# Kernel optimization log

Measured on AMD Instinct MI355X. Metric: run time of the kernel, lower is better.

The kernel has to match this reference:

```python
import jax, jax.numpy as jnp
import numpy as np

B, N, C = 8, 1024, 768
H, D = 12, 64
SCALE = D ** -0.5
EPS = 1e-5

def layernorm(x, g, b):
    mu = jnp.mean(x, axis=-1, keepdims=True)
    var = jnp.var(x, axis=-1, keepdims=True)
    return (x - mu) * jax.lax.rsqrt(var + EPS) * g + b

def setup_inputs() -> dict:
    key = jax.random.key(0)
    ks = jax.random.split(key, 5)
    return {
        "x": jax.random.normal(ks[0], (B, N, C), jnp.float32),
        "qkv_w": jax.random.normal(ks[1], (3 * C, C), jnp.float32) * 0.02,
        "qkv_b": jax.random.normal(ks[2], (3 * C,), jnp.float32) * 0.02,
        "qn_g": jnp.ones((D,), jnp.float32),
        "qn_b": jnp.zeros((D,), jnp.float32),
        "kn_g": jnp.ones((D,), jnp.float32),
        "kn_b": jnp.zeros((D,), jnp.float32),
        "proj_w": jax.random.normal(ks[3], (C, C), jnp.float32) * 0.02,
        "proj_b": jnp.zeros((C,), jnp.float32),
    }

def reference(x, qkv_w, qkv_b, qn_g, qn_b, kn_g, kn_b, proj_w, proj_b):
    # qkv projection: [B,N,3C] -> [3,B,H,N,D]
    qkv = jnp.einsum('bnc,oc->bno', x, qkv_w) + qkv_b
    qkv = qkv.reshape(B, N, 3, H, D).transpose(2, 0, 3, 1, 4)
    q, k, v = qkv[0], qkv[1], qkv[2]
    q = layernorm(q, qn_g, qn_b) * SCALE
    k = layernorm(k, kn_g, kn_b)
    # explicit attention matrix [B,H,N,N] (module stores it)
    attn = jax.nn.softmax(jnp.einsum('bhqd,bhkd->bhqk', q, k), axis=-1)
    out = jnp.einsum('bhqk,bhkd->bhqd', attn, v)
    out = out.transpose(0, 2, 1, 3).reshape(B, N, C)
    out = jnp.einsum('bnc,oc->bno', out, proj_w) + proj_b
    return out
```

## Files before the change

### kernel.cpp

```cpp
#include <hip/hip_runtime.h>
#include <cstdint>

#define Bz 8
#define Nn 1024
#define Cc 768
#define Hh 12
#define Dd 64
#define C3 2304
#define BN 8192

constexpr float EPS = 1e-5f;
constexpr float QSCALE = 0.125f * 1.44269504088896340736f;

typedef __attribute__((ext_vector_type(8))) short bf16x8;
typedef _Float16 f16x8 __attribute__((ext_vector_type(8)));
typedef __attribute__((ext_vector_type(4))) float f32x4;
typedef __attribute__((ext_vector_type(16))) float f32x16;

__device__ __forceinline__ short f2b(float f) {
    union { float f; unsigned u; } x; x.f = f;
    unsigned r = x.u + 0x7FFFu + ((x.u >> 16) & 1u);
    return (short)(r >> 16);
}
__device__ __forceinline__ unsigned cvtpk(float a, float b) {
    unsigned r;
    asm("v_cvt_pk_bf16_f32 %0, %1, %2" : "=v"(r) : "v"(a), "v"(b));
    return r;
}

__device__ __forceinline__ f32x4 MFMAH(f16x8 a, f16x8 b, f32x4 c) {
    return __builtin_amdgcn_mfma_f32_16x16x32_f16(a, b, c, 0, 0, 0);
}
__device__ __forceinline__ f32x16 MFMA32(bf16x8 a, bf16x8 b, f32x16 c) {
    return __builtin_amdgcn_mfma_f32_32x32x16_bf16(a, b, c, 0, 0, 0);
}
__device__ __forceinline__ f16x8 ldf16(const _Float16* p) { return *(const f16x8*)p; }
__device__ __forceinline__ void gld16(const void* g, void* l) {
    __builtin_amdgcn_global_load_lds((const __attribute__((address_space(1))) unsigned int*)g,
                                     (__attribute__((address_space(3))) unsigned int*)(l),
                                     16, 0, 0);
}

__global__ __launch_bounds__(256) void cvt_all(
    const float* __restrict__ x, const float* __restrict__ wq, const float* __restrict__ wp,
    _Float16* __restrict__ xh, _Float16* __restrict__ wqh, _Float16* __restrict__ wph)
{
    const int n1 = BN * Cc / 8, n2 = n1 + C3 * Cc / 8, n3 = n2 + Cc * Cc / 8;
    int i = blockIdx.x * 256 + threadIdx.x;
    const float* s; _Float16* d; int off;
    if (i < n1)      { s = x;  d = xh;  off = i; }
    else if (i < n2) { s = wq; d = wqh; off = i - n1; }
    else if (i < n3) { s = wp; d = wph; off = i - n2; }
    else return;
    float4 a = *(const float4*)(s + (size_t)off * 8);
    float4 b = *(const float4*)(s + (size_t)off * 8 + 4);
    f16x8 o;
    o[0] = (_Float16)a.x; o[1] = (_Float16)a.y; o[2] = (_Float16)a.z; o[3] = (_Float16)a.w;
    o[4] = (_Float16)b.x; o[5] = (_Float16)b.y; o[6] = (_Float16)b.z; o[7] = (_Float16)b.w;
    *(f16x8*)(d + (size_t)off * 8) = o;
}

template<int EPI>
__global__ __launch_bounds__(256, 4) void gemm_f16(
    const _Float16* __restrict__ A,
    const _Float16* __restrict__ W,
    const float* __restrict__ bias,
    float* __restrict__ Out,
    short* __restrict__ qp, short* __restrict__ kp, short* __restrict__ vp,
    const float* __restrict__ qg, const float* __restrict__ qb,
    const float* __restrict__ kg, const float* __restrict__ kb,
    int nx)
{
    __shared__ _Float16 As[128 * 64];
    __shared__ _Float16 Bs[128 * 64];
    const int tid = threadIdx.x;
    const int lane = tid & 63;
    const int w = tid >> 6;
    const int wr = w >> 1, wc = w & 1;
    const int l15 = lane & 15, l4 = lane >> 4;
    const int lr = lane >> 3;
    const int lslot = lane & 7;

    const int chunk = gridDim.x >> 3;
    const int wg = (blockIdx.x & 7) * chunk + (blockIdx.x >> 3);
    const int by = wg / nx;
    int bx = wg % nx;
    if (by & 1) bx = nx - 1 - bx;
    const int m0 = by * 128;
    const int n0 = bx * 128;

    auto stage = [&](int kt) {
        const int k0 = kt * 64;
#pragma unroll
        for (int j = 0; j < 8; ++j) {
            int i = w * 8 + j;
            int isA = (i < 16);
            int ib = isA ? i : i - 16;
            int row = ib * 8 + lr;
            int gslot = lslot ^ (row & 7);
            const _Float16* src = (isA ? A + (size_t)(m0 + row) * 768
                                       : W + (size_t)(n0 + row) * 768) + k0 + gslot * 8;
            _Float16* dst = (isA ? As : Bs) + ib * 512;
            gld16(src, dst);
        }
    };

    f32x4 acc[4][4];
#pragma unroll
    for (int mi = 0; mi < 4; ++mi)
#pragma unroll
        for (int ni = 0; ni < 4; ++ni) { acc[mi][ni][0]=0.f; acc[mi][ni][1]=0.f; acc[mi][ni][2]=0.f; acc[mi][ni][3]=0.f; }

    stage(0);
    for (int kt = 0; kt < 12; ++kt) {
        __syncthreads();
#pragma unroll
        for (int ks = 0; ks < 2; ++ks) {
            f16x8 af[4], bfr[4];
#pragma unroll
            for (int mi = 0; mi < 4; ++mi) {
                int row = wr * 64 + mi * 16 + l15;
                int slot = (ks * 4 + l4) ^ (row & 7);
                af[mi] = ldf16(&As[row * 64 + slot * 8]);
            }
#pragma unroll
            for (int ni = 0; ni < 4; ++ni) {
                int row = wc * 64 + ni * 16 + l15;
                int slot = (ks * 4 + l4) ^ (row & 7);
                bfr[ni] = ldf16(&Bs[row * 64 + slot * 8]);
            }
#pragma unroll
            for (int mi = 0; mi < 4; ++mi)
#pragma unroll
                for (int ni = 0; ni < 4; ++ni)
                    acc[mi][ni] = MFMAH(af[mi], bfr[ni], acc[mi][ni]);
        }
        __syncthreads();
        if (kt < 11) stage(kt + 1);
    }

    if (EPI == 0) {
#pragma unroll
        for (int mi = 0; mi < 4; ++mi)
#pragma unroll
            for (int r = 0; r < 4; ++r) {
                int row = m0 + wr * 64 + mi * 16 + l4 * 4 + r;
#pragma unroll
                for (int ni = 0; ni < 4; ++ni) {
                    int col = n0 + wc * 64 + ni * 16 + l15;
                    Out[(size_t)row * Cc + col] = acc[mi][ni][r] + bias[col];
                }
            }
    } else {
        const int ncol0 = n0 + wc * 64;
        const int type = ncol0 / Cc;
        const int h = (ncol0 % Cc) >> 6;
        const float* gptr = (type == 0) ? qg : kg;
        const float* bptr = (type == 0) ? qb : kb;
        float biasv[4], gv[4], bv[4];
#pragma unroll
        for (int ni = 0; ni < 4; ++ni) {
            int d = ni * 16 + l15;
            biasv[ni] = bias[ncol0 + d];
            if (type < 2) { gv[ni] = gptr[d]; bv[ni] = bptr[d]; }
        }
        short* plane = (type == 0) ? qp : (type == 1) ? kp : vp;
#pragma unroll
        for (int mi = 0; mi < 4; ++mi)
#pragma unroll
            for (int r = 0; r < 4; ++r) {
                float v[4];
#pragma unroll
                for (int ni = 0; ni < 4; ++ni) v[ni] = acc[mi][ni][r] + biasv[ni];
                int row = m0 + wr * 64 + mi * 16 + l4 * 4 + r;
                size_t base = ((size_t)row * Hh + h) * 64;
                if (type < 2) {
                    float s = v[0] + v[1] + v[2] + v[3];
#pragma unroll
                    for (int off = 1; off < 16; off <<= 1) s += __shfl_xor(s, off);
                    float mu = s * (1.0f / 64.0f);
                    float s2 = 0.f;
#pragma unroll
                    for (int ni = 0; ni < 4; ++ni) { float dv = v[ni] - mu; s2 += dv * dv; }
#pragma unroll
                    for (int off = 1; off < 16; off <<= 1) s2 += __shfl_xor(s2, off);
                    float inv = rsqrtf(s2 * (1.0f / 64.0f) + EPS);
#pragma unroll
                    for (int ni = 0; ni < 4; ++ni) {
                        float rr = (v[ni] - mu) * inv * gv[ni] + bv[ni];
                        if (type == 0) rr *= QSCALE;
                        plane[base + ni * 16 + l15] = f2b(rr);
                    }
                } else {
#pragma unroll
                    for (int ni = 0; ni < 4; ++ni)
                        plane[base + ni * 16 + l15] = f2b(v[ni]);
                }
            }
    }
}

__global__ __launch_bounds__(256, 4) void flash_attn_mfma(
    const short* __restrict__ qp, const short* __restrict__ kp, const short* __restrict__ vp,
    _Float16* __restrict__ att)
{
    __shared__ short kls[2][64 * 64];
    __shared__ short vtl[2][64 * 64];
    const int tid = threadIdx.x;
    const int lane = tid & 63;
    const int w = tid >> 6;
    const int l31 = lane & 31;
    const int hi = lane >> 5;
    const int lr = lane >> 3;
    const int lslot = lane & 7;
    const int bid = (blockIdx.x & 7) * 96 + (blockIdx.x >> 3);
    const int qt = bid & 7;
    const int bh = bid >> 3;
    const int h = bh % Hh;
    const int b = bh / Hh;
    const int q0 = qt * 128;
    const size_t hbase = ((size_t)b * Nn * Hh + h) * 64;
    const int n0v = (tid & 31) * 2, d0v = (tid >> 5) * 8;
    const int khalf = n0v & 31;
    const int t2v = n0v >> 5;
    const int ksig = khalf ^ ((((khalf >> 2) ^ (khalf >> 3)) & 1) * 12);
    const int colv = t2v * 32 + ksig;

    bf16x8 qf[4];
    {
        const short* qsrc = qp + hbase + (size_t)(q0 + w * 32 + l31) * 768 + hi * 8;
#pragma unroll
        for (int ds = 0; ds < 4; ++ds)
            qf[ds] = *(const bf16x8*)(qsrc + ds * 16);
    }

    auto kstage = [&](int kt, int buf) {
#pragma unroll
        for (int i = 0; i < 2; ++i) {
            int row = i * 32 + w * 8 + lr;
            gld16(kp + hbase + (size_t)(kt * 64 + row) * 768 + (lslot ^ lr) * 8,
                  &kls[buf][(i * 32 + w * 8) * 64]);
        }
    };
    auto vcommit = [&](int buf, bf16x8 a0, bf16x8 a1) {
#pragma unroll
        for (int j = 0; j < 8; ++j) {
            int d = d0v + j;
            int fv = (d ^ (d >> 3)) & 7;
            unsigned pku = (unsigned short)a0[j] | ((unsigned)(unsigned short)a1[j] << 16);
            *(unsigned*)&vtl[buf][d * 64 + (((colv >> 3) ^ fv) << 3) + (colv & 7)] = pku;
        }
    };

    kstage(0, 0);
    {
        const short* s0 = vp + hbase + (size_t)n0v * 768 + d0v;
        vcommit(0, *(const bf16x8*)s0, *(const bf16x8*)(s0 + 768));
    }
    __syncthreads();

    f32x16 o0, o1;
#pragma unroll
    for (int i = 0; i < 16; ++i) { o0[i] = 0.f; o1[i] = 0.f; }
    float lrun = 0.f;

    for (int kt = 0; kt < 16; ++kt) {
        const int cur = kt & 1, nxt = cur ^ 1;
        bf16x8 va0, va1;
        if (kt < 15) {
            kstage(kt + 1, nxt);
            const short* s0 = vp + hbase + (size_t)((kt + 1) * 64 + n0v) * 768 + d0v;
            va0 = *(const bf16x8*)s0;
            va1 = *(const bf16x8*)(s0 + 768);
        }
        unsigned pk[2][8];
#pragma unroll
        for (int t2 = 0; t2 < 2; ++t2) {
            f32x16 st;
#pragma unroll
            for (int i = 0; i < 16; ++i) st[i] = 0.f;
            const int row = t2 * 32 + l31;
            __builtin_amdgcn_s_setprio(1);
#pragma unroll
            for (int ds = 0; ds < 4; ++ds) {
                bf16x8 kf = *(const bf16x8*)&kls[cur][row * 64 + (((ds * 2 + hi) ^ (row & 7)) << 3)];
                st = MFMA32(kf, qf[ds], st);
            }
            __builtin_amdgcn_s_setprio(0);
#pragma unroll
            for (int i = 0; i < 16; ++i) st[i] = exp2f(st[i]);
            {
                float s01 = (st[0] + st[1]) + (st[2] + st[3]);
                float s23 = (st[4] + st[5]) + (st[6] + st[7]);
                float s45 = (st[8] + st[9]) + (st[10] + st[11]);
                float s67 = (st[12] + st[13]) + (st[14] + st[15]);
                lrun += (s01 + s23) + (s45 + s67);
            }
#pragma unroll
            for (int i = 0; i < 8; ++i) pk[t2][i] = cvtpk(st[2 * i], st[2 * i + 1]);
        }
        __builtin_amdgcn_s_setprio(1);
#pragma unroll
        for (int t2 = 0; t2 < 2; ++t2)
#pragma unroll
            for (int c = 0; c < 2; ++c) {
                union { bf16x8 v; unsigned u[4]; } a;
                a.u[0] = pk[t2][c * 4 + 0]; a.u[1] = pk[t2][c * 4 + 1];
                a.u[2] = pk[t2][c * 4 + 2]; a.u[3] = pk[t2][c * 4 + 3];
#pragma unroll
                for (int nt = 0; nt < 2; ++nt) {
                    int r = nt * 32 + l31;
                    int fv = (r ^ (r >> 3)) & 7;
                    bf16x8 vf = *(const bf16x8*)&vtl[cur][r * 64 + (((t2 * 4 + c * 2 + hi) ^ fv) << 3)];
                    if (nt == 0) o0 = MFMA32(a.v, vf, o0);
                    else         o1 = MFMA32(a.v, vf, o1);
                }
            }
        __builtin_amdgcn_s_setprio(0);
        if (kt < 15) vcommit(nxt, va0, va1);
        __syncthreads();
    }

    lrun += __shfl_xor(lrun, 32);
    float linv = 1.0f / lrun;
#pragma unroll
    for (int r = 0; r < 16; ++r) {
        int qr = (r & 3) + 8 * (r >> 2) + 4 * hi;
        float invr = __shfl(linv, qr);
        int row = q0 + w * 32 + qr;
        _Float16* dst = att + (size_t)(b * Nn + row) * Cc + h * 64 + l31;
        dst[0]  = (_Float16)(o0[r] * invr);
        dst[32] = (_Float16)(o1[r] * invr);
    }
}

extern "C" void kernel_launch(void* const* d_in, const int* in_sizes, int n_in,
                              void* d_out, int out_size, void* d_ws, size_t ws_size,
                              hipStream_t stream)
{
    const float* x      = (const float*)d_in[0];
    const float* qkv_w  = (const float*)d_in[1];
    const float* qkv_b  = (const float*)d_in[2];
    const float* qn_g   = (const float*)d_in[3];
    const float* qn_b   = (const float*)d_in[4];
    const float* kn_g   = (const float*)d_in[5];
    const float* kn_b   = (const float*)d_in[6];
    const float* proj_w = (const float*)d_in[7];
    const float* proj_b = (const float*)d_in[8];
    float* out = (float*)d_out;

    char* ws = (char*)d_ws;
    short*    qp  = (short*)(ws);
    short*    kp  = (short*)(ws + 12582912);
    short*    vp  = (short*)(ws + 25165824);
    _Float16* att = (_Float16*)(ws + 37748736);
    _Float16* xh  = (_Float16*)(ws + 50331648);
    _Float16* wqh = (_Float16*)(ws + 62914560);
    _Float16* wph = (_Float16*)(ws + 66453504);

    {
        const int n3 = BN * Cc / 8 + C3 * Cc / 8 + Cc * Cc / 8;
        cvt_all<<<(n3 + 255) / 256, 256, 0, stream>>>(x, qkv_w, proj_w, xh, wqh, wph);
    }
    gemm_f16<1><<<(BN / 128) * (C3 / 128), 256, 0, stream>>>(
        xh, wqh, qkv_b, nullptr, qp, kp, vp, qn_g, qn_b, kn_g, kn_b, C3 / 128);
    flash_attn_mfma<<<Bz * Hh * 8, 256, 0, stream>>>(qp, kp, vp, att);
    gemm_f16<0><<<(BN / 128) * (Cc / 128), 256, 0, stream>>>(
        att, wph, proj_b, out, nullptr, nullptr, nullptr, nullptr, nullptr, nullptr, nullptr, Cc / 128);
}
```

Baseline: 126.5 us.

## Halve attention query tile to 64 rows and single-buffer K in LDS

The flash attention kernel now uses 128-thread blocks covering 64 query rows each, doubling the grid, with each thread loading twice as much V. K staging goes to a single LDS buffer refilled after a mid-iteration barrier once both score MFMAs have consumed it, and the two score tiles are computed together. The aim is more blocks for better CU fill and lower LDS use per block. The cost is that K/V tiles are reloaded by twice as many blocks, K prefetch overlaps less with compute, and there is an extra barrier per iteration.

Result: no change. 126.8 us (+0.2%).

```diff
diff --git a/kernel.cpp b/kernel.cpp
--- a/kernel.cpp
+++ b/kernel.cpp
@@ -200,11 +200,11 @@
     }
 }
 
-__global__ __launch_bounds__(256, 4) void flash_attn_mfma(
+__global__ __launch_bounds__(128, 3) void flash_attn_mfma(
     const short* __restrict__ qp, const short* __restrict__ kp, const short* __restrict__ vp,
     _Float16* __restrict__ att)
 {
-    __shared__ short kls[2][64 * 64];
+    __shared__ short kls[64 * 64];
     __shared__ short vtl[2][64 * 64];
     const int tid = threadIdx.x;
     const int lane = tid & 63;
@@ -213,14 +213,14 @@
     const int hi = lane >> 5;
     const int lr = lane >> 3;
     const int lslot = lane & 7;
-    const int bid = (blockIdx.x & 7) * 96 + (blockIdx.x >> 3);
-    const int qt = bid & 7;
-    const int bh = bid >> 3;
+    const int bid = (blockIdx.x & 7) * 192 + (blockIdx.x >> 3);
+    const int qt = bid & 15;
+    const int bh = bid >> 4;
     const int h = bh % Hh;
     const int b = bh / Hh;
-    const int q0 = qt * 128;
+    const int q0 = qt * 64;
     const size_t hbase = ((size_t)b * Nn * Hh + h) * 64;
-    const int n0v = (tid & 31) * 2, d0v = (tid >> 5) * 8;
+    const int n0v = (tid & 31) * 2, d0v = (tid >> 5) * 16;
     const int khalf = n0v & 31;
     const int t2v = n0v >> 5;
     const int ksig = khalf ^ ((((khalf >> 2) ^ (khalf >> 3)) & 1) * 12);
@@ -234,28 +234,39 @@
             qf[ds] = *(const bf16x8*)(qsrc + ds * 16);
     }
 
-    auto kstage = [&](int kt, int buf) {
-#pragma unroll
-        for (int i = 0; i < 2; ++i) {
-            int row = i * 32 + w * 8 + lr;
+    auto kstage = [&](int kt) {
+#pragma unroll
+        for (int j = 0; j < 4; ++j) {
+            int i = w * 4 + j;
+            int row = i * 8 + lr;
             gld16(kp + hbase + (size_t)(kt * 64 + row) * 768 + (lslot ^ lr) * 8,
-                  &kls[buf][(i * 32 + w * 8) * 64]);
+                  &kls[i * 512]);
         }
     };
-    auto vcommit = [&](int buf, bf16x8 a0, bf16x8 a1) {
-#pragma unroll
-        for (int j = 0; j < 8; ++j) {
-            int d = d0v + j;
-            int fv = (d ^ (d >> 3)) & 7;
-            unsigned pku = (unsigned short)a0[j] | ((unsigned)(unsigned short)a1[j] << 16);
-            *(unsigned*)&vtl[buf][d * 64 + (((colv >> 3) ^ fv) << 3) + (colv & 7)] = pku;
-        }
+    auto vload = [&](int kt, bf16x8* va) {
+        const short* s0 = vp + hbase + (size_t)(kt * 64 + n0v) * 768 + d0v;
+        va[0] = *(const bf16x8*)s0;
+        va[1] = *(const bf16x8*)(s0 + 8);
+        va[2] = *(const bf16x8*)(s0 + 768);
+        va[3] = *(const bf16x8*)(s0 + 768 + 8);
     };
-
-    kstage(0, 0);
+    auto vcommit = [&](int buf, const bf16x8* va) {
+#pragma unroll
+        for (int g = 0; g < 2; ++g)
+#pragma unroll
+            for (int j = 0; j < 8; ++j) {
+                int d = d0v + g * 8 + j;
+                int fv = (d ^ (d >> 3)) & 7;
+                unsigned pku = (unsigned short)va[g][j] | ((unsigned)(unsigned short)va[g + 2][j] << 16);
+                *(unsigned*)&vtl[buf][d * 64 + (((colv >> 3) ^ fv) << 3) + (colv & 7)] = pku;
+            }
+    };
+
+    kstage(0);
     {
-        const short* s0 = vp + hbase + (size_t)n0v * 768 + d0v;
-        vcommit(0, *(const bf16x8*)s0, *(const bf16x8*)(s0 + 768));
+        bf16x8 va[4];
+        vload(0, va);
+        vcommit(0, va);
     }
     __syncthreads();
 
@@ -266,39 +277,36 @@
 
     for (int kt = 0; kt < 16; ++kt) {
         const int cur = kt & 1, nxt = cur ^ 1;
-        bf16x8 va0, va1;
-        if (kt < 15) {
-            kstage(kt + 1, nxt);
-            const short* s0 = vp + hbase + (size_t)((kt + 1) * 64 + n0v) * 768 + d0v;
-            va0 = *(const bf16x8*)s0;
-            va1 = *(const bf16x8*)(s0 + 768);
-        }
+        bf16x8 va[4];
+        if (kt < 15) vload(kt + 1, va);
+        f32x16 st0, st1;
+#pragma unroll
+        for (int i = 0; i < 16; ++i) { st0[i] = 0.f; st1[i] = 0.f; }
+        __builtin_amdgcn_s_setprio(1);
+#pragma unroll
+        for (int ds = 0; ds < 4; ++ds) {
+            bf16x8 kf0 = *(const bf16x8*)&kls[l31 * 64 + (((ds * 2 + hi) ^ (l31 & 7)) << 3)];
+            bf16x8 kf1 = *(const bf16x8*)&kls[(32 + l31) * 64 + (((ds * 2 + hi) ^ ((32 + l31) & 7)) << 3)];
+            st0 = MFMA32(kf0, qf[ds], st0);
+            st1 = MFMA32(kf1, qf[ds], st1);
+        }
+        __builtin_amdgcn_s_setprio(0);
+        __builtin_amdgcn_s_barrier();
+        if (kt < 15) kstage(kt + 1);
         unsigned pk[2][8];
 #pragma unroll
-        for (int t2 = 0; t2 < 2; ++t2) {
-            f32x16 st;
-#pragma unroll
-            for (int i = 0; i < 16; ++i) st[i] = 0.f;
-            const int row = t2 * 32 + l31;
-            __builtin_amdgcn_s_setprio(1);
-#pragma unroll
-            for (int ds = 0; ds < 4; ++ds) {
-                bf16x8 kf = *(const bf16x8*)&kls[cur][row * 64 + (((ds * 2 + hi) ^ (row & 7)) << 3)];
-                st = MFMA32(kf, qf[ds], st);
-            }
-            __builtin_amdgcn_s_setprio(0);
-#pragma unroll
-            for (int i = 0; i < 16; ++i) st[i] = exp2f(st[i]);
-            {
-                float s01 = (st[0] + st[1]) + (st[2] + st[3]);
-                float s23 = (st[4] + st[5]) + (st[6] + st[7]);
-                float s45 = (st[8] + st[9]) + (st[10] + st[11]);
-                float s67 = (st[12] + st[13]) + (st[14] + st[15]);
-                lrun += (s01 + s23) + (s45 + s67);
-            }
-#pragma unroll
-            for (int i = 0; i < 8; ++i) pk[t2][i] = cvtpk(st[2 * i], st[2 * i + 1]);
-        }
+        for (int i = 0; i < 16; ++i) st0[i] = exp2f(st0[i]);
+#pragma unroll
+        for (int i = 0; i < 16; ++i) st1[i] = exp2f(st1[i]);
+        {
+            float a0 = 0.f, a1 = 0.f;
+#pragma unroll
+            for (int i = 0; i < 16; ++i) { a0 += st0[i]; a1 += st1[i]; }
+            lrun += a0 + a1;
+        }
+#pragma unroll
+        for (int i = 0; i < 8; ++i) { pk[0][i] = cvtpk(st0[2 * i], st0[2 * i + 1]);
+                                      pk[1][i] = cvtpk(st1[2 * i], st1[2 * i + 1]); }
         __builtin_amdgcn_s_setprio(1);
 #pragma unroll
         for (int t2 = 0; t2 < 2; ++t2)
@@ -317,7 +325,7 @@
                 }
             }
         __builtin_amdgcn_s_setprio(0);
-        if (kt < 15) vcommit(nxt, va0, va1);
+        if (kt < 15) vcommit(nxt, va);
         __syncthreads();
     }
 
@@ -364,7 +372,7 @@
     }
     gemm_f16<1><<<(BN / 128) * (C3 / 128), 256, 0, stream>>>(
         xh, wqh, qkv_b, nullptr, qp, kp, vp, qn_g, qn_b, kn_g, kn_b, C3 / 128);
-    flash_attn_mfma<<<Bz * Hh * 8, 256, 0, stream>>>(qp, kp, vp, att);
+    flash_attn_mfma<<<Bz * Hh * 16, 128, 0, stream>>>(qp, kp, vp, att);
     gemm_f16<0><<<(BN / 128) * (Cc / 128), 256, 0, stream>>>(
         att, wph, proj_b, out, nullptr, nullptr, nullptr, nullptr, nullptr, nullptr, nullptr, Cc / 128);
 }
```

## Fuse fp32-to-fp16 conversion of x into QKV GEMM A-tile loading

Applied to the files above, without the earlier changes.

Removes the separate conversion pass over the activation x. The QKV GEMM now loads fp32 rows into registers, prefetching one k-tile ahead during compute, and packs them to fp16 into the swizzled LDS tile. The pack uses round-toward-zero, where the old conversion rounded to nearest. This saves an extra read and write of x, but the GEMM now reads twice as many bytes per A tile, once per column tile. The A path also moves from direct-to-LDS loads to register staging, which raises register pressure and lowers the occupancy hint from 4 to 3.

Measured after the change: 175.1 us. 1.38x slower.

```diff
diff --git a/kernel.cpp b/kernel.cpp
--- a/kernel.cpp
+++ b/kernel.cpp
@@ -27,6 +27,11 @@
     asm("v_cvt_pk_bf16_f32 %0, %1, %2" : "=v"(r) : "v"(a), "v"(b));
     return r;
 }
+__device__ __forceinline__ unsigned pkrtz(float a, float b) {
+    auto h = __builtin_amdgcn_cvt_pkrtz(a, b);
+    union { decltype(h) v; unsigned u; } x; x.v = h;
+    return x.u;
+}
 
 __device__ __forceinline__ f32x4 MFMAH(f16x8 a, f16x8 b, f32x4 c) {
     return __builtin_amdgcn_mfma_f32_16x16x32_f16(a, b, c, 0, 0, 0);
@@ -41,16 +46,15 @@
                                      16, 0, 0);
 }
 
-__global__ __launch_bounds__(256) void cvt_all(
-    const float* __restrict__ x, const float* __restrict__ wq, const float* __restrict__ wp,
-    _Float16* __restrict__ xh, _Float16* __restrict__ wqh, _Float16* __restrict__ wph)
+__global__ __launch_bounds__(256) void cvt_w(
+    const float* __restrict__ wq, const float* __restrict__ wp,
+    _Float16* __restrict__ wqh, _Float16* __restrict__ wph)
 {
-    const int n1 = BN * Cc / 8, n2 = n1 + C3 * Cc / 8, n3 = n2 + Cc * Cc / 8;
+    const int n1 = C3 * Cc / 8, n2 = n1 + Cc * Cc / 8;
     int i = blockIdx.x * 256 + threadIdx.x;
     const float* s; _Float16* d; int off;
-    if (i < n1)      { s = x;  d = xh;  off = i; }
-    else if (i < n2) { s = wq; d = wqh; off = i - n1; }
-    else if (i < n3) { s = wp; d = wph; off = i - n2; }
+    if (i < n1)      { s = wq; d = wqh; off = i; }
+    else if (i < n2) { s = wp; d = wph; off = i - n1; }
     else return;
     float4 a = *(const float4*)(s + (size_t)off * 8);
     float4 b = *(const float4*)(s + (size_t)off * 8 + 4);
@@ -61,8 +65,8 @@
 }
 
 template<int EPI>
-__global__ __launch_bounds__(256, 4) void gemm_f16(
-    const _Float16* __restrict__ A,
+__global__ __launch_bounds__(256, 3) void gemm_f16(
+    const void* __restrict__ Ain,
     const _Float16* __restrict__ W,
     const float* __restrict__ bias,
     float* __restrict__ Out,
@@ -80,6 +84,10 @@
     const int l15 = lane & 15, l4 = lane >> 4;
     const int lr = lane >> 3;
     const int lslot = lane & 7;
+    const _Float16* A16 = (const _Float16*)Ain;
+    const float*    A32 = (const float*)Ain;
+    const int arow = tid >> 1;
+    const int akq  = (tid & 1) * 32;
 
     const int chunk = gridDim.x >> 3;
     const int wg = (blockIdx.x & 7) * chunk + (blockIdx.x >> 3);
@@ -89,19 +97,41 @@
     const int m0 = by * 128;
     const int n0 = bx * 128;
 
-    auto stage = [&](int kt) {
+    auto stageB = [&](int kt) {
         const int k0 = kt * 64;
 #pragma unroll
-        for (int j = 0; j < 8; ++j) {
-            int i = w * 8 + j;
-            int isA = (i < 16);
-            int ib = isA ? i : i - 16;
+        for (int j = 0; j < 4; ++j) {
+            int ib = w * 4 + j;
             int row = ib * 8 + lr;
             int gslot = lslot ^ (row & 7);
-            const _Float16* src = (isA ? A + (size_t)(m0 + row) * 768
-                                       : W + (size_t)(n0 + row) * 768) + k0 + gslot * 8;
-            _Float16* dst = (isA ? As : Bs) + ib * 512;
-            gld16(src, dst);
+            gld16(W + (size_t)(n0 + row) * 768 + k0 + gslot * 8, Bs + ib * 512);
+        }
+    };
+    auto stageA16 = [&](int kt) {
+        const int k0 = kt * 64;
+#pragma unroll
+        for (int j = 0; j < 4; ++j) {
+            int ib = w * 4 + j;
+            int row = ib * 8 + lr;
+            int gslot = lslot ^ (row & 7);
+            gld16(A16 + (size_t)(m0 + row) * 768 + k0 + gslot * 8, As + ib * 512);
+        }
+    };
+    auto aload = [&](int kt, float4* ar) {
+        const float* src = A32 + (size_t)(m0 + arow) * 768 + kt * 64 + akq;
+#pragma unroll
+        for (int j = 0; j < 8; ++j) ar[j] = ((const float4*)src)[j];
+    };
+    auto acommit = [&](const float4* ar) {
+#pragma unroll
+        for (int i = 0; i < 4; ++i) {
+            union { unsigned u[4]; f16x8 v; } u;
+            u.u[0] = pkrtz(ar[2 * i].x,     ar[2 * i].y);
+            u.u[1] = pkrtz(ar[2 * i].z,     ar[2 * i].w);
+            u.u[2] = pkrtz(ar[2 * i + 1].x, ar[2 * i + 1].y);
+            u.u[3] = pkrtz(ar[2 * i + 1].z, ar[2 * i + 1].w);
+            int s = ((akq >> 3) + i) ^ (arow & 7);
+            *(f16x8*)&As[arow * 64 + s * 8] = u.v;
         }
     };
 
@@ -111,9 +141,14 @@
 #pragma unroll
         for (int ni = 0; ni < 4; ++ni) { acc[mi][ni][0]=0.f; acc[mi][ni][1]=0.f; acc[mi][ni][2]=0.f; acc[mi][ni][3]=0.f; }
 
-    stage(0);
+    if (EPI == 1) { float4 ar0[8]; aload(0, ar0); acommit(ar0); }
+    else stageA16(0);
+    stageB(0);
+
+    float4 ar[8];
     for (int kt = 0; kt < 12; ++kt) {
         __syncthreads();
+        if (EPI == 1 && kt < 11) aload(kt + 1, ar);
 #pragma unroll
         for (int ks = 0; ks < 2; ++ks) {
             f16x8 af[4], bfr[4];
@@ -136,7 +171,10 @@
                     acc[mi][ni] = MFMAH(af[mi], bfr[ni], acc[mi][ni]);
         }
         __syncthreads();
-        if (kt < 11) stage(kt + 1);
+        if (kt < 11) {
+            if (EPI == 1) acommit(ar); else stageA16(kt + 1);
+            stageB(kt + 1);
+        }
     }
 
     if (EPI == 0) {
@@ -354,16 +392,15 @@
     short*    kp  = (short*)(ws + 12582912);
     short*    vp  = (short*)(ws + 25165824);
     _Float16* att = (_Float16*)(ws + 37748736);
-    _Float16* xh  = (_Float16*)(ws + 50331648);
     _Float16* wqh = (_Float16*)(ws + 62914560);
     _Float16* wph = (_Float16*)(ws + 66453504);
 
     {
-        const int n3 = BN * Cc / 8 + C3 * Cc / 8 + Cc * Cc / 8;
-        cvt_all<<<(n3 + 255) / 256, 256, 0, stream>>>(x, qkv_w, proj_w, xh, wqh, wph);
+        const int n2 = C3 * Cc / 8 + Cc * Cc / 8;
+        cvt_w<<<(n2 + 255) / 256, 256, 0, stream>>>(qkv_w, proj_w, wqh, wph);
     }
     gemm_f16<1><<<(BN / 128) * (C3 / 128), 256, 0, stream>>>(
-        xh, wqh, qkv_b, nullptr, qp, kp, vp, qn_g, qn_b, kn_g, kn_b, C3 / 128);
+        x, wqh, qkv_b, nullptr, qp, kp, vp, qn_g, qn_b, kn_g, kn_b, C3 / 128);
     flash_attn_mfma<<<Bz * Hh * 8, 256, 0, stream>>>(qp, kp, vp, att);
     gemm_f16<0><<<(BN / 128) * (Cc / 128), 256, 0, stream>>>(
         att, wph, proj_b, out, nullptr, nullptr, nullptr, nullptr, nullptr, nullptr, nullptr, Cc / 128);
```
